# Kernel tuning notes

Measured on AMD Instinct MI355X. Metric: run time of the kernel, lower is better.

## Reference

```python
import jax, jax.numpy as jnp
import numpy as np

NUM_HEADS = 12
HEAD_DIM = 64  # dim=768 // 12
SCALE = HEAD_DIM ** (-0.5)  # NOTE: original divides q by this -> multiplies by sqrt(head_dim)


def setup_inputs() -> dict:
    key = jax.random.key(0)
    k1, k2, k3 = jax.random.split(key, 3)
    B, N, C = 1, 4096, 768
    x = jax.random.normal(k1, (B, N, C), dtype=jnp.float32)
    qkv_w = jax.random.normal(k2, (3 * C, C), dtype=jnp.float32) * 0.01
    qkv_b = jnp.zeros((3 * C,), dtype=jnp.float32)
    proj_w = jax.random.normal(k3, (C, C), dtype=jnp.float32) * 0.01
    proj_b = jnp.zeros((C,), dtype=jnp.float32)
    return {"x": x, "qkv_w": qkv_w, "qkv_b": qkv_b, "proj_w": proj_w, "proj_b": proj_b}


def reference(x, qkv_w, qkv_b, proj_w, proj_b):
    B, N, C = x.shape
    H, D = NUM_HEADS, HEAD_DIM
    # qkv projection: [B,N,3C]
    qkv = x @ qkv_w.T + qkv_b
    qkv = qkv.reshape(B, N, 3, H, D).transpose(2, 0, 3, 1, 4)  # [3,B,H,N,D]
    q, k, v = qkv[0], qkv[1], qkv[2]
    # Faithful quirk: q / scale with scale = D**-0.5 => logits scaled by sqrt(D)
    attn = jnp.einsum('bhnd,bhmd->bhnm', q / SCALE, k)  # [B,H,N,N]
    attn = jax.nn.softmax(attn, axis=-1)
    # dropout omitted (eval mode / deterministic reference)
    out = jnp.einsum('bhnm,bhmd->bhnd', attn, v)  # [B,H,N,D]
    out = out.transpose(0, 2, 1, 3).reshape(B, N, C)
    out = out @ proj_w.T + proj_b
    return out
```

## Files before the change

### kernel.cpp

```cpp
#include <hip/hip_runtime.h>


typedef short bf16x8 __attribute__((ext_vector_type(8)));
typedef float f32x4 __attribute__((ext_vector_type(4)));
typedef unsigned short u16;
typedef unsigned int u32;

__device__ __forceinline__ u16 f2bf(float f) {
  u32 u = __float_as_uint(f);
  u = (u + 0x7fffu + ((u >> 16) & 1u)) >> 16;
  return (u16)u;
}

__device__ __forceinline__ u32 cvtpk(float a, float b) {
  u32 r;
  asm("v_cvt_pk_bf16_f32 %0, %1, %2" : "=v"(r) : "v"(a), "v"(b));
  return r;
}

__device__ __forceinline__ void gload16(const void* g, void* l) {
  __builtin_amdgcn_global_load_lds(
      (const __attribute__((address_space(1))) unsigned int*)g,
      (__attribute__((address_space(3))) unsigned int*)l, 16, 0, 0);
}

__device__ __forceinline__ void pl32swap(u32& x, u32& y) {
  asm("v_permlane32_swap_b32 %0, %1" : "+v"(x), "+v"(y));
}
__device__ __forceinline__ void pl16swap(u32& x, u32& y) {
  asm("v_permlane16_swap_b32 %0, %1" : "+v"(x), "+v"(y));
}

__global__ void cast3(const float* __restrict__ a, int na4,
                      const float* __restrict__ b, int nb4,
                      const float* __restrict__ c, int nc4,
                      u16* __restrict__ oa, u16* __restrict__ obp, u16* __restrict__ oc) {
  int i = blockIdx.x * blockDim.x + threadIdx.x;
  const float* src;
  u16* dst;
  int j = i;
  if (i < na4) { src = a; dst = oa; }
  else if (i < na4 + nb4) { src = b; dst = obp; j = i - na4; }
  else if (i < na4 + nb4 + nc4) { src = c; dst = oc; j = i - na4 - nb4; }
  else return;
  float4 v = ((const float4*)src)[j];
  ushort4 o;
  o.x = f2bf(v.x); o.y = f2bf(v.y); o.z = f2bf(v.z); o.w = f2bf(v.w);
  ((ushort4*)dst)[j] = o;
}

template <int MODE>
__global__ __launch_bounds__(256, 2) void gemm_bt(
    const u16* __restrict__ A, const u16* __restrict__ B,
    const float* __restrict__ bias,
    u16* __restrict__ qb, u16* __restrict__ kbuf, u16* __restrict__ vb,
    float* __restrict__ outp, int K, int N) {
  constexpr int TM = (MODE == 1) ? 64 : 128;
  constexpr int MI = TM / 32;
  __shared__ __align__(16) u16 As[2][TM * 32];
  __shared__ __align__(16) u16 Bs[2][128 * 32];
  const int tid = threadIdx.x, lane = tid & 63, w = tid >> 6;
  const int wr = w >> 1, wc = w & 1, quad = lane >> 4, l15 = lane & 15;
  const int m0 = blockIdx.y * TM, n0 = blockIdx.x * 128;

  f32x4 acc[MI][4];
#pragma unroll
  for (int i = 0; i < MI; ++i)
#pragma unroll
    for (int j = 0; j < 4; ++j) acc[i][j] = (f32x4){0.f, 0.f, 0.f, 0.f};

  auto stage = [&](int k0, int sb) {
#pragma unroll
    for (int i = 0; i < TM / 64; ++i) {
      int chunk = i * 256 + tid;
      int row = chunk >> 2, kc = chunk & 3;
      gload16(A + (size_t)(m0 + row) * K + k0 + kc * 8, (char*)&As[sb][0] + chunk * 16);
    }
#pragma unroll
    for (int i = 0; i < 2; ++i) {
      int chunk = i * 256 + tid;
      int row = chunk >> 2, kc = chunk & 3;
      gload16(B + (size_t)(n0 + row) * K + k0 + kc * 8, (char*)&Bs[sb][0] + chunk * 16);
    }
  };

  stage(0, 0);

  int ib = 0;
  for (int k0 = 0; k0 < K; k0 += 32, ib ^= 1) {
    __syncthreads();
    if (k0 + 32 < K) stage(k0 + 32, ib ^ 1);

    bf16x8 af[MI], bfr[4];
#pragma unroll
    for (int mi = 0; mi < MI; ++mi)
      af[mi] = *(const bf16x8*)&As[ib][(wr * (TM / 2) + mi * 16 + l15) * 32 + quad * 8];
#pragma unroll
    for (int ni = 0; ni < 4; ++ni)
      bfr[ni] = *(const bf16x8*)&Bs[ib][(wc * 64 + ni * 16 + l15) * 32 + quad * 8];
#pragma unroll
    for (int mi = 0; mi < MI; ++mi)
#pragma unroll
      for (int ni = 0; ni < 4; ++ni)
        acc[mi][ni] = __builtin_amdgcn_mfma_f32_16x16x32_bf16(af[mi], bfr[ni], acc[mi][ni], 0, 0, 0);
  }

#pragma unroll
  for (int mi = 0; mi < MI; ++mi) {
    int row = m0 + wr * (TM / 2) + mi * 16 + quad * 4;
#pragma unroll
    for (int ni = 0; ni < 4; ++ni) {
      int col = n0 + wc * 64 + ni * 16 + l15;
      float bv = bias[col];
      if (MODE == 0) {
        int t = col / 768;
        int rem = col - t * 768;
        int hh = rem >> 6, d = rem & 63;
        if (t == 2) {
          u16* dst = vb + (size_t)hh * 64 * 4096 + (size_t)d * 4096 + row;
          ushort4 pk;
          pk.x = f2bf(acc[mi][ni][0] + bv);
          pk.y = f2bf(acc[mi][ni][1] + bv);
          pk.z = f2bf(acc[mi][ni][2] + bv);
          pk.w = f2bf(acc[mi][ni][3] + bv);
          *(ushort4*)dst = pk;
        } else {
          u16* dst = (t == 0 ? qb : kbuf) + (size_t)hh * 4096 * 64 + d;
          float sc = (t == 0) ? 11.541560327111707f : 1.f;
#pragma unroll
          for (int r = 0; r < 4; ++r)
            dst[(size_t)(row + r) * 64] = f2bf((acc[mi][ni][r] + bv) * sc);
        }
      } else {
#pragma unroll
        for (int r = 0; r < 4; ++r)
          outp[(size_t)(row + r) * N + col] = acc[mi][ni][r] + bv;
      }
    }
  }
}

__global__ __launch_bounds__(256, 3) void flash_attn(
    const u16* __restrict__ qb, const u16* __restrict__ kb,
    const u16* __restrict__ vtg, u16* __restrict__ ob) {
  __shared__ __align__(16) u16 Ks[2][64 * 64];
  __shared__ __align__(16) u16 Vs[2][64 * 64];

  const int b = blockIdx.x;
  const int g = (b & 7) * 96 + (b >> 3);
  const int h = g >> 6;
  const int q0 = (g & 63) * 64;

  const int tid = threadIdx.x, lane = tid & 63, w = tid >> 6;
  const int quad = lane >> 4, l15 = lane & 15;
  const int qh2 = w >> 1, kh = w & 1;
  const u16* qptr = qb + (size_t)h * 4096 * 64;
  const u16* kptr = kb + (size_t)h * 4096 * 64;
  const u16* vptr = vtg + (size_t)h * 64 * 4096;
  const int sw = l15 & 7;
  const int u0 = (quad ^ sw) * 8;
  const int u1 = ((quad + 4) ^ sw) * 8;
  const int uv = (((kh << 2) + quad) ^ sw) * 8;

  int c0 = w * 64 + lane, c1 = 256 + w * 64 + lane;
  int r0s = c0 >> 3, j0s = ((c0 & 7) ^ (r0s & 7)) * 8;
  int r1s = c1 >> 3, j1s = ((c1 & 7) ^ (r1s & 7)) * 8;

  bf16x8 qf[2][2];
#pragma unroll
  for (int qt = 0; qt < 2; ++qt)
#pragma unroll
    for (int c = 0; c < 2; ++c)
      qf[qt][c] = *(const bf16x8*)&qptr[(size_t)(q0 + qh2 * 32 + qt * 16 + l15) * 64 + c * 32 + quad * 8];

  f32x4 oacc[2][4];
  f32x4 lacc[2];
#pragma unroll
  for (int qt = 0; qt < 2; ++qt) {
    lacc[qt] = (f32x4){0.f, 0.f, 0.f, 0.f};
#pragma unroll
    for (int dt = 0; dt < 4; ++dt) oacc[qt][dt] = (f32x4){0.f, 0.f, 0.f, 0.f};
  }
  const f32x4 zero4 = (f32x4){0.f, 0.f, 0.f, 0.f};
  bf16x8 onesf;
#pragma unroll
  for (int i = 0; i < 8; ++i) onesf[i] = (short)0x3F80;

  bf16x8 pfprev[2], vprev[4];

  gload16(kptr + (size_t)r0s * 64 + j0s, (char*)&Ks[0][0] + c0 * 16);
  gload16(kptr + (size_t)r1s * 64 + j1s, (char*)&Ks[0][0] + c1 * 16);
  gload16(vptr + (size_t)r0s * 4096 + j0s, (char*)&Vs[0][0] + c0 * 16);
  gload16(vptr + (size_t)r1s * 4096 + j1s, (char*)&Vs[0][0] + c1 * 16);

  const u16* ks0 = kptr + (size_t)(64 + r0s) * 64 + j0s;
  const u16* ks1 = kptr + (size_t)(64 + r1s) * 64 + j1s;
  const u16* vs0 = vptr + (size_t)r0s * 4096 + 64 + j0s;
  const u16* vs1 = vptr + (size_t)r1s * 4096 + 64 + j1s;

  auto body = [&](int t, int buf) {
    __syncthreads();
    if (t < 63) {
      gload16(ks0, (char*)&Ks[buf ^ 1][0] + c0 * 16);
      gload16(ks1, (char*)&Ks[buf ^ 1][0] + c1 * 16);
      gload16(vs0, (char*)&Vs[buf ^ 1][0] + c0 * 16);
      gload16(vs1, (char*)&Vs[buf ^ 1][0] + c1 * 16);
      ks0 += 64 * 64; ks1 += 64 * 64; vs0 += 64; vs1 += 64;
    }

    bf16x8 kf[2][2];
#pragma unroll
    for (int mt = 0; mt < 2; ++mt) {
      const u16* kr = &Ks[buf][((kh << 5) + mt * 16 + l15) * 64];
      kf[mt][0] = *(const bf16x8*)(kr + u0);
      kf[mt][1] = *(const bf16x8*)(kr + u1);
    }

    __builtin_amdgcn_s_setprio(1);
    if (t > 0) {
#pragma unroll
      for (int qt = 0; qt < 2; ++qt) {
#pragma unroll
        for (int dt = 0; dt < 4; ++dt)
          oacc[qt][dt] = __builtin_amdgcn_mfma_f32_16x16x32_bf16(pfprev[qt], vprev[dt], oacc[qt][dt], 0, 0, 0);
        lacc[qt] = __builtin_amdgcn_mfma_f32_16x16x32_bf16(pfprev[qt], onesf, lacc[qt], 0, 0, 0);
      }
    }

    f32x4 st[2][2];
#pragma unroll
    for (int mt = 0; mt < 2; ++mt)
#pragma unroll
      for (int qt = 0; qt < 2; ++qt) {
        f32x4 z = __builtin_amdgcn_mfma_f32_16x16x32_bf16(kf[mt][0], qf[qt][0], zero4, 0, 0, 0);
        st[mt][qt] = __builtin_amdgcn_mfma_f32_16x16x32_bf16(kf[mt][1], qf[qt][1], z, 0, 0, 0);
      }
    __builtin_amdgcn_s_setprio(0);

#pragma unroll
    for (int dt = 0; dt < 4; ++dt)
      vprev[dt] = *(const bf16x8*)(&Vs[buf][(dt * 16 + l15) * 64] + uv);

#pragma unroll
    for (int qt = 0; qt < 2; ++qt) {
      float p00 = __builtin_amdgcn_exp2f(st[0][qt][0]);
      float p01 = __builtin_amdgcn_exp2f(st[0][qt][1]);
      float p02 = __builtin_amdgcn_exp2f(st[0][qt][2]);
      float p03 = __builtin_amdgcn_exp2f(st[0][qt][3]);
      float p10 = __builtin_amdgcn_exp2f(st[1][qt][0]);
      float p11 = __builtin_amdgcn_exp2f(st[1][qt][1]);
      float p12 = __builtin_amdgcn_exp2f(st[1][qt][2]);
      float p13 = __builtin_amdgcn_exp2f(st[1][qt][3]);
      u32 x0 = cvtpk(p00, p01), x1 = cvtpk(p02, p03);
      u32 y0 = cvtpk(p10, p11), y1 = cvtpk(p12, p13);
      pl32swap(x0, y0); pl16swap(x0, y0);
      pl32swap(x1, y1); pl16swap(x1, y1);
      union { u32 u[4]; bf16x8 v; } pu;
      pu.u[0] = x0; pu.u[1] = x1; pu.u[2] = y0; pu.u[3] = y1;
      pfprev[qt] = pu.v;
    }
  };

  for (int tt = 0; tt < 32; ++tt) {
    body(2 * tt, 0);
    body(2 * tt + 1, 1);
  }

#pragma unroll
  for (int qt = 0; qt < 2; ++qt) {
#pragma unroll
    for (int dt = 0; dt < 4; ++dt)
      oacc[qt][dt] = __builtin_amdgcn_mfma_f32_16x16x32_bf16(pfprev[qt], vprev[dt], oacc[qt][dt], 0, 0, 0);
    lacc[qt] = __builtin_amdgcn_mfma_f32_16x16x32_bf16(pfprev[qt], onesf, lacc[qt], 0, 0, 0);
  }

  __syncthreads();
  float* ored = (float*)&Ks[0][0];
  float* lred = (float*)&Vs[0][0];
  if (kh == 1) {
#pragma unroll
    for (int qt = 0; qt < 2; ++qt) {
#pragma unroll
      for (int dt = 0; dt < 4; ++dt)
        *(f32x4*)&ored[((((qh2 * 2 + qt) * 4 + dt) * 64) + lane) * 4] = oacc[qt][dt];
      if (l15 == 0) {
#pragma unroll
        for (int r = 0; r < 4; ++r)
          lred[(qh2 * 2 + qt) * 16 + quad * 4 + r] = lacc[qt][r];
      }
    }
  }
  __syncthreads();
  if (kh == 0) {
#pragma unroll
    for (int qt = 0; qt < 2; ++qt) {
      f32x4 linv;
#pragma unroll
      for (int r = 0; r < 4; ++r)
        linv[r] = 1.f / (lacc[qt][r] + lred[(qh2 * 2 + qt) * 16 + quad * 4 + r]);
#pragma unroll
      for (int dt = 0; dt < 4; ++dt) {
        f32x4 oo = *(const f32x4*)&ored[((((qh2 * 2 + qt) * 4 + dt) * 64) + lane) * 4];
        int row = q0 + qh2 * 32 + qt * 16 + quad * 4;
        u16* op = ob + (size_t)row * 768 + h * 64 + dt * 16 + l15;
        op[0]       = f2bf((oacc[qt][dt][0] + oo[0]) * linv[0]);
        op[768]     = f2bf((oacc[qt][dt][1] + oo[1]) * linv[1]);
        op[2 * 768] = f2bf((oacc[qt][dt][2] + oo[2]) * linv[2]);
        op[3 * 768] = f2bf((oacc[qt][dt][3] + oo[3]) * linv[3]);
      }
    }
  }
}

extern "C" void kernel_launch(void* const* d_in, const int* in_sizes, int n_in,
                              void* d_out, int out_size, void* d_ws, size_t ws_size,
                              hipStream_t stream) {
  const float* x      = (const float*)d_in[0];
  const float* qkv_w  = (const float*)d_in[1];
  const float* qkv_b  = (const float*)d_in[2];
  const float* proj_w = (const float*)d_in[3];
  const float* proj_b = (const float*)d_in[4];
  float* out = (float*)d_out;

  const int N = 4096, C = 768, H = 12, D = 64, C3 = 2304;
  char* ws = (char*)d_ws;
  size_t off = 0;
  u16* xb    = (u16*)(ws + off); off += (size_t)N * C * 2;
  u16* wqkv  = (u16*)(ws + off); off += (size_t)C3 * C * 2;
  u16* wproj = (u16*)(ws + off); off += (size_t)C * C * 2;
  u16* qbuf  = (u16*)(ws + off); off += (size_t)H * N * D * 2;
  u16* kbuf  = (u16*)(ws + off); off += (size_t)H * N * D * 2;
  u16* vbuf  = (u16*)(ws + off); off += (size_t)H * N * D * 2;
  u16* aob = xb;

  const int na4 = N * C / 4, nb4 = C3 * C / 4, nc4 = C * C / 4;
  int ntot = na4 + nb4 + nc4;
  cast3<<<(ntot + 255) / 256, 256, 0, stream>>>(x, na4, qkv_w, nb4, proj_w, nc4, xb, wqkv, wproj);

  dim3 g1(C3 / 128, N / 128);
  gemm_bt<0><<<g1, 256, 0, stream>>>(xb, wqkv, qkv_b, qbuf, kbuf, vbuf, nullptr, C, C3);

  flash_attn<<<768, 256, 0, stream>>>(qbuf, kbuf, vbuf, aob);

  dim3 g3(C / 128, N / 64);
  gemm_bt<1><<<g3, 256, 0, stream>>>(aob, wproj, proj_b, nullptr, nullptr, nullptr, out, C, C);
}
```

Before: 118.7 us.

## Fuse fp32-to-bf16 casts into GEMM tile staging, drop cast kernel

Removes the separate cast kernel that turned x, qkv_w and proj_w into bf16. The GEMMs now read fp32 directly, convert with v_cvt_pk_bf16_f32 and write to LDS through registers instead of using async global_load_lds. This saves a launch and a full round trip of the casted data through memory. In exchange each GEMM reads twice the bytes per tile, weights are re-converted by every block that loads them, and staging becomes synchronous, so it was moved after the fragment reads to keep some overlap.

Result: slower. 132.2 us (+11.4%).

```diff
diff --git a/kernel.cpp b/kernel.cpp
--- a/kernel.cpp
+++ b/kernel.cpp
@@ -31,27 +31,9 @@
   asm("v_permlane16_swap_b32 %0, %1" : "+v"(x), "+v"(y));
 }
 
-__global__ void cast3(const float* __restrict__ a, int na4,
-                      const float* __restrict__ b, int nb4,
-                      const float* __restrict__ c, int nc4,
-                      u16* __restrict__ oa, u16* __restrict__ obp, u16* __restrict__ oc) {
-  int i = blockIdx.x * blockDim.x + threadIdx.x;
-  const float* src;
-  u16* dst;
-  int j = i;
-  if (i < na4) { src = a; dst = oa; }
-  else if (i < na4 + nb4) { src = b; dst = obp; j = i - na4; }
-  else if (i < na4 + nb4 + nc4) { src = c; dst = oc; j = i - na4 - nb4; }
-  else return;
-  float4 v = ((const float4*)src)[j];
-  ushort4 o;
-  o.x = f2bf(v.x); o.y = f2bf(v.y); o.z = f2bf(v.z); o.w = f2bf(v.w);
-  ((ushort4*)dst)[j] = o;
-}
-
 template <int MODE>
 __global__ __launch_bounds__(256, 2) void gemm_bt(
-    const u16* __restrict__ A, const u16* __restrict__ B,
+    const void* __restrict__ Ain, const void* __restrict__ Bin,
     const float* __restrict__ bias,
     u16* __restrict__ qb, u16* __restrict__ kbuf, u16* __restrict__ vb,
     float* __restrict__ outp, int K, int N) {
@@ -63,6 +45,10 @@
   const int wr = w >> 1, wc = w & 1, quad = lane >> 4, l15 = lane & 15;
   const int m0 = blockIdx.y * TM, n0 = blockIdx.x * 128;
 
+  const float* Af32 = (const float*)Ain;
+  const u16*   Abf  = (const u16*)Ain;
+  const float* Bf32 = (const float*)Bin;
+
   f32x4 acc[MI][4];
 #pragma unroll
   for (int i = 0; i < MI; ++i)
@@ -70,17 +56,31 @@
     for (int j = 0; j < 4; ++j) acc[i][j] = (f32x4){0.f, 0.f, 0.f, 0.f};
 
   auto stage = [&](int k0, int sb) {
-#pragma unroll
-    for (int i = 0; i < TM / 64; ++i) {
-      int chunk = i * 256 + tid;
+    if (MODE == 0) {
+#pragma unroll
+      for (int i = 0; i < 2; ++i) {
+        int chunk = i * 256 + tid;
+        int row = chunk >> 2, kc = chunk & 3;
+        const float* s = Af32 + (size_t)(m0 + row) * K + k0 + kc * 8;
+        float4 a = *(const float4*)s;
+        float4 b2 = *(const float4*)(s + 4);
+        uint4 pk = {cvtpk(a.x, a.y), cvtpk(a.z, a.w), cvtpk(b2.x, b2.y), cvtpk(b2.z, b2.w)};
+        *(uint4*)((char*)&As[sb][0] + chunk * 16) = pk;
+      }
+    } else {
+      int chunk = tid;
       int row = chunk >> 2, kc = chunk & 3;
-      gload16(A + (size_t)(m0 + row) * K + k0 + kc * 8, (char*)&As[sb][0] + chunk * 16);
+      gload16(Abf + (size_t)(m0 + row) * K + k0 + kc * 8, (char*)&As[sb][0] + chunk * 16);
     }
 #pragma unroll
     for (int i = 0; i < 2; ++i) {
       int chunk = i * 256 + tid;
       int row = chunk >> 2, kc = chunk & 3;
-      gload16(B + (size_t)(n0 + row) * K + k0 + kc * 8, (char*)&Bs[sb][0] + chunk * 16);
+      const float* s = Bf32 + (size_t)(n0 + row) * K + k0 + kc * 8;
+      float4 a = *(const float4*)s;
+      float4 b2 = *(const float4*)(s + 4);
+      uint4 pk = {cvtpk(a.x, a.y), cvtpk(a.z, a.w), cvtpk(b2.x, b2.y), cvtpk(b2.z, b2.w)};
+      *(uint4*)((char*)&Bs[sb][0] + chunk * 16) = pk;
     }
   };
 
@@ -89,7 +89,6 @@
   int ib = 0;
   for (int k0 = 0; k0 < K; k0 += 32, ib ^= 1) {
     __syncthreads();
-    if (k0 + 32 < K) stage(k0 + 32, ib ^ 1);
 
     bf16x8 af[MI], bfr[4];
 #pragma unroll
@@ -98,6 +97,9 @@
 #pragma unroll
     for (int ni = 0; ni < 4; ++ni)
       bfr[ni] = *(const bf16x8*)&Bs[ib][(wc * 64 + ni * 16 + l15) * 32 + quad * 8];
+
+    if (k0 + 32 < K) stage(k0 + 32, ib ^ 1);
+
 #pragma unroll
     for (int mi = 0; mi < MI; ++mi)
 #pragma unroll
@@ -325,23 +327,18 @@
   const int N = 4096, C = 768, H = 12, D = 64, C3 = 2304;
   char* ws = (char*)d_ws;
   size_t off = 0;
-  u16* xb    = (u16*)(ws + off); off += (size_t)N * C * 2;
-  u16* wqkv  = (u16*)(ws + off); off += (size_t)C3 * C * 2;
-  u16* wproj = (u16*)(ws + off); off += (size_t)C * C * 2;
+  u16* aob   = (u16*)(ws + off); off += (size_t)N * C * 2;
   u16* qbuf  = (u16*)(ws + off); off += (size_t)H * N * D * 2;
   u16* kbuf  = (u16*)(ws + off); off += (size_t)H * N * D * 2;
   u16* vbuf  = (u16*)(ws + off); off += (size_t)H * N * D * 2;
-  u16* aob = xb;
-
-  const int na4 = N * C / 4, nb4 = C3 * C / 4, nc4 = C * C / 4;
-  int ntot = na4 + nb4 + nc4;
-  cast3<<<(ntot + 255) / 256, 256, 0, stream>>>(x, na4, qkv_w, nb4, proj_w, nc4, xb, wqkv, wproj);
 
   dim3 g1(C3 / 128, N / 128);
-  gemm_bt<0><<<g1, 256, 0, stream>>>(xb, wqkv, qkv_b, qbuf, kbuf, vbuf, nullptr, C, C3);
+  gemm_bt<0><<<g1, 256, 0, stream>>>((const void*)x, (const void*)qkv_w, qkv_b,
+                                     qbuf, kbuf, vbuf, nullptr, C, C3);
 
   flash_attn<<<768, 256, 0, stream>>>(qbuf, kbuf, vbuf, aob);
 
   dim3 g3(C / 128, N / 64);
-  gemm_bt<1><<<g3, 256, 0, stream>>>(aob, wproj, proj_b, nullptr, nullptr, nullptr, out, C, C);
-}
+  gemm_bt<1><<<g3, 256, 0, stream>>>((const void*)aob, (const void*)proj_w, proj_b,
+                                     nullptr, nullptr, nullptr, out, C, C);
+}
```
